# Performance work log

Measured on AMD Instinct MI355X. Metric: run time of the kernel, lower is better.

## Reference

```python
import jax, jax.numpy as jnp
import numpy as np
import math

D = 1024  # output_dim (power of 2)
IN = 1024  # input dim
CAP = int(math.log2(D))  # number of butterfly stages


def _gen_indices(s):
    """Static FFT-butterfly index lists (numpy, computed at trace time)."""
    def ind_s(k):
        if k == 0:
            return [np.array([1, 0])]
        temp = np.arange(2 ** k)
        list0 = [np.concatenate([temp + 2 ** k, temp])]
        list1 = ind_s(k - 1)
        for i in range(k):
            list0.append(np.concatenate([list1[i], list1[i] + 2 ** k]))
        return list0

    t = ind_s(int(math.log2(s // 2)))
    cap = int(math.log2(s))
    ind_exe = [np.asarray(t[i], dtype=np.int32) for i in range(cap)]
    ind_param = []
    for i in range(cap):
        ind = np.concatenate([np.arange(0, s, 2 ** i) + j for j in range(2 ** i)]).astype(np.int32)
        ind_param.append(ind)
    return ind_exe, ind_param


IND_EXE, IND_PARAM = _gen_indices(D)


def setup_inputs() -> dict:
    key = jax.random.key(0)
    ks = jax.random.split(key, 9)
    B = 8192
    x = jax.random.normal(ks[0], (B, IN), dtype=jnp.float32)
    state = jax.random.normal(ks[1], (B, D), dtype=jnp.float32)
    theta = jax.random.uniform(ks[2], (CAP, D // 2), minval=-3.14, maxval=3.14, dtype=jnp.float32)
    U = jax.random.uniform(ks[3], (IN, 3 * D), minval=-0.01, maxval=0.01, dtype=jnp.float32)
    W_r = jax.random.uniform(ks[4], (D, D), minval=-0.01, maxval=0.01, dtype=jnp.float32)
    W_g = jax.random.uniform(ks[5], (D, D), minval=-0.01, maxval=0.01, dtype=jnp.float32)
    bias_r = jnp.full((D,), 2.0, dtype=jnp.float32)
    bias_g = jnp.zeros((D,), dtype=jnp.float32)
    bias_c = jnp.full((D,), 0.01, dtype=jnp.float32)
    return {"x": x, "state": state, "theta": theta, "U": U, "W_r": W_r,
            "W_g": W_g, "bias_r": bias_r, "bias_g": bias_g, "bias_c": bias_c}


def reference(x, state, theta, U, W_r, W_g, bias_r, bias_g, bias_c):
    # fft_param: rotation coefficients, permuted by the static ind_param lists
    cos_list = jnp.concatenate([jnp.cos(theta), jnp.cos(theta)], axis=1)   # [CAP, D]
    sin_list = jnp.concatenate([jnp.sin(theta), -jnp.sin(theta)], axis=1)  # [CAP, D]
    v1 = jnp.stack([cos_list[i][IND_PARAM[i]] for i in range(CAP)])  # [CAP, D]
    v2 = jnp.stack([sin_list[i][IND_PARAM[i]] for i in range(CAP)])  # [CAP, D]

    Ux = x @ U                                   # [B, 3D]
    U_cx, U_rx, U_gx = jnp.split(Ux, 3, axis=1)  # each [B, D]
    r = jax.nn.sigmoid(U_rx + state @ W_r + bias_r)
    g = jax.nn.sigmoid(U_gx + state @ W_g + bias_g)

    # butterfly orthogonal rotation of the state
    h = state
    for i in range(CAP):
        h = h * v1[i] + (h * v2[i])[:, IND_EXE[i]]

    # modReLU
    pre = r * h + U_cx
    c = jnp.sign(pre) * jax.nn.relu(jnp.abs(pre) + 0.001 + bias_c)

    out = g * state + (1.0 - g) * c
    return out
```

## Files before the change

### kernel.cpp

```cpp
#include <hip/hip_runtime.h>
#include <hip/hip_bf16.h>
#include <stdint.h>


typedef __bf16 bf16x8 __attribute__((ext_vector_type(8)));
typedef __bf16 bf16x4 __attribute__((ext_vector_type(4)));
typedef __bf16 bf16x2 __attribute__((ext_vector_type(2)));
typedef float f32x4 __attribute__((ext_vector_type(4)));

#define B_ROWS 8192

__device__ __forceinline__ void async16(__bf16* lds, const __hip_bfloat16* g) {
    __builtin_amdgcn_global_load_lds((const __attribute__((address_space(1))) void*)g,
                                     (__attribute__((address_space(3))) void*)lds,
                                     16, 0, 0);
}

__global__ __launch_bounds__(256) void prep_all(const float* __restrict__ x,
                                                const float* __restrict__ state,
                                                const float* __restrict__ theta,
                                                const float* __restrict__ U,
                                                const float* __restrict__ Wr,
                                                const float* __restrict__ Wg,
                                                __hip_bfloat16* __restrict__ xs,
                                                __hip_bfloat16* __restrict__ Wt0,
                                                __hip_bfloat16* __restrict__ Wt12,
                                                float* __restrict__ v1,
                                                float* __restrict__ v2) {
    __shared__ float tile[32][33];
    const int id = blockIdx.x;
    if (id < 8192) {
        const int row = id;
        const int col = threadIdx.x * 8;
        const float* src = (col < 1024) ? (x + (size_t)row * 1024 + col)
                                        : (state + (size_t)row * 1024 + (col - 1024));
        float4 a = *(const float4*)src;
        float4 b = *(const float4*)(src + 4);
        bf16x8 v;
        v[0] = (__bf16)a.x; v[1] = (__bf16)a.y; v[2] = (__bf16)a.z; v[3] = (__bf16)a.w;
        v[4] = (__bf16)b.x; v[5] = (__bf16)b.y; v[6] = (__bf16)b.z; v[7] = (__bf16)b.w;
        *(bf16x8*)((__bf16*)xs + (size_t)row * 2048 + col) = v;
    } else if (id < 13312) {
        const int wid = id - 8192;
        const float* src; int srcN, scol, sk;
        __hip_bfloat16* dst; int dstStride, dn, dk;
        if (wid < 1024) {
            int nx = wid & 31, ky = wid >> 5;
            src = U; srcN = 3072; scol = nx * 32; sk = ky * 32;
            dst = Wt0; dstStride = 1024; dn = nx * 32; dk = ky * 32;
        } else {
            int id2 = wid - 1024;
            int nx = id2 & 63, ky = id2 >> 6;
            int n0 = nx * 32, k0 = ky * 32;
            dst = Wt12; dstStride = 2048; dn = n0; dk = k0;
            if (k0 < 1024)      { src = U;  srcN = 3072; scol = 1024 + n0; sk = k0; }
            else if (n0 < 1024) { src = Wr; srcN = 1024; scol = n0;        sk = k0 - 1024; }
            else                { src = Wg; srcN = 1024; scol = n0 - 1024; sk = k0 - 1024; }
        }
        const int tx = threadIdx.x & 31, ty = threadIdx.x >> 5;
#pragma unroll
        for (int s = 0; s < 4; ++s)
            tile[ty + s * 8][tx] = src[(size_t)(sk + ty + s * 8) * srcN + scol + tx];
        __syncthreads();
#pragma unroll
        for (int s = 0; s < 4; ++s)
            dst[(size_t)(dn + ty + s * 8) * dstStride + dk + tx] = __float2bfloat16(tile[tx][ty + s * 8]);
    } else {
        int idx = (id - 13312) * 256 + threadIdx.x;
        int i = idx >> 10;
        int j = idx & 1023;
        int Q = 1024 >> i;
        int j0 = j / Q;
        int m = j & (Q - 1);
        int q = (m << i) + j0;
        float th = theta[i * 512 + (q & 511)];
        float c = cosf(th);
        float s = sinf(th);
        v1[idx] = c;
        v2[idx] = (q < 512) ? s : -s;
    }
}

__global__ __launch_bounds__(512, 4) void gemm_fused(const __hip_bfloat16* __restrict__ xs,
                                                     const __hip_bfloat16* __restrict__ Wt0,
                                                     const __hip_bfloat16* __restrict__ Wt12,
                                                     const float* __restrict__ bias_r,
                                                     const float* __restrict__ bias_g,
                                                     __hip_bfloat16* __restrict__ P) {
    __shared__ __align__(16) __bf16 As[128 * 32];
    __shared__ __align__(16) __bf16 Bs1[128 * 32];
    __shared__ __align__(16) __bf16 Bs2[128 * 32];

    const int nt = blockIdx.x;
    const int mt = blockIdx.y;
    const int mBase = mt * 128;

    const int t = threadIdx.x;
    const int lane = t & 63;
    const int wv = t >> 6;
    const int wm = wv & 1;
    const int wn = wv >> 1;
    const int r0 = lane & 15;
    const int gq = lane >> 4;

    const int srow = t >> 2;
    const int sjj = ((t & 3) ^ ((srow >> 1) & 3)) * 8;

    const __hip_bfloat16* A = xs + (size_t)mBase * 2048;

    if (nt < 8) {
        const int c0 = nt * 128;
        const __hip_bfloat16* B1 = Wt12 + (size_t)c0 * 2048;
        const __hip_bfloat16* B2 = Wt12 + (size_t)(1024 + c0) * 2048;

        f32x4 accr[4][2], accg[4][2];
        const f32x4 zero = {0.f, 0.f, 0.f, 0.f};
#pragma unroll
        for (int i = 0; i < 4; ++i)
#pragma unroll
            for (int j = 0; j < 2; ++j) { accr[i][j] = zero; accg[i][j] = zero; }

        for (int k0 = 0; k0 < 2048; k0 += 32) {
            size_t off = (size_t)srow * 2048 + k0 + sjj;
            async16(&As[t * 8], A + off);
            async16(&Bs1[t * 8], B1 + off);
            async16(&Bs2[t * 8], B2 + off);
            __syncthreads();

            bf16x8 af[4], b1[2], b2[2];
#pragma unroll
            for (int i = 0; i < 4; ++i) {
                int row = wm * 64 + i * 16 + r0;
                int cc = row * 4 + (gq ^ ((row >> 1) & 3));
                af[i] = *reinterpret_cast<const bf16x8*>(&As[cc * 8]);
            }
#pragma unroll
            for (int j = 0; j < 2; ++j) {
                int row = wn * 32 + j * 16 + r0;
                int cc = row * 4 + (gq ^ ((row >> 1) & 3));
                b1[j] = *reinterpret_cast<const bf16x8*>(&Bs1[cc * 8]);
                b2[j] = *reinterpret_cast<const bf16x8*>(&Bs2[cc * 8]);
            }
#pragma unroll
            for (int i = 0; i < 4; ++i)
#pragma unroll
                for (int j = 0; j < 2; ++j) {
                    accr[i][j] = __builtin_amdgcn_mfma_f32_16x16x32_bf16(af[i], b1[j], accr[i][j], 0, 0, 0);
                    accg[i][j] = __builtin_amdgcn_mfma_f32_16x16x32_bf16(af[i], b2[j], accg[i][j], 0, 0, 0);
                }
            __syncthreads();
        }

#pragma unroll
        for (int i = 0; i < 4; ++i) {
#pragma unroll
            for (int j = 0; j < 2; ++j) {
#pragma unroll
                for (int reg = 0; reg < 4; ++reg) {
                    int row = mBase + wm * 64 + i * 16 + gq * 4 + reg;
                    int c = c0 + wn * 32 + j * 16 + r0;
                    float zr = 1.0f / (1.0f + __expf(-(accr[i][j][reg] + bias_r[c])));
                    float zg = 1.0f / (1.0f + __expf(-(accg[i][j][reg] + bias_g[c])));
                    bf16x2 pk;
                    pk[0] = (__bf16)zr;
                    pk[1] = (__bf16)zg;
                    *(bf16x2*)((__bf16*)P + (size_t)row * 3072 + 1024 + 2 * c) = pk;
                }
            }
        }
    } else {
        const int c0 = (nt - 8) * 128;
        const __hip_bfloat16* Bb = Wt0 + (size_t)c0 * 1024;

        f32x4 acc[4][2];
        const f32x4 zero = {0.f, 0.f, 0.f, 0.f};
#pragma unroll
        for (int i = 0; i < 4; ++i)
#pragma unroll
            for (int j = 0; j < 2; ++j) acc[i][j] = zero;

        for (int k0 = 0; k0 < 1024; k0 += 32) {
            async16(&As[t * 8], A + (size_t)srow * 2048 + k0 + sjj);
            async16(&Bs1[t * 8], Bb + (size_t)srow * 1024 + k0 + sjj);
            __syncthreads();

            bf16x8 af[4], bf[2];
#pragma unroll
            for (int i = 0; i < 4; ++i) {
                int row = wm * 64 + i * 16 + r0;
                int cc = row * 4 + (gq ^ ((row >> 1) & 3));
                af[i] = *reinterpret_cast<const bf16x8*>(&As[cc * 8]);
            }
#pragma unroll
            for (int j = 0; j < 2; ++j) {
                int row = wn * 32 + j * 16 + r0;
                int cc = row * 4 + (gq ^ ((row >> 1) & 3));
                bf[j] = *reinterpret_cast<const bf16x8*>(&Bs1[cc * 8]);
            }
#pragma unroll
            for (int i = 0; i < 4; ++i)
#pragma unroll
                for (int j = 0; j < 2; ++j)
                    acc[i][j] = __builtin_amdgcn_mfma_f32_16x16x32_bf16(af[i], bf[j], acc[i][j], 0, 0, 0);
            __syncthreads();
        }

#pragma unroll
        for (int i = 0; i < 4; ++i) {
#pragma unroll
            for (int j = 0; j < 2; ++j) {
#pragma unroll
                for (int reg = 0; reg < 4; ++reg) {
                    int row = mBase + wm * 64 + i * 16 + gq * 4 + reg;
                    int c = c0 + wn * 32 + j * 16 + r0;
                    P[(size_t)row * 3072 + c] = __float2bfloat16(acc[i][j][reg]);
                }
            }
        }
    }
}

__global__ __launch_bounds__(256) void fuse_kernel(const float* __restrict__ state,
                                                   const __hip_bfloat16* __restrict__ P,
                                                   const float* __restrict__ v1,
                                                   const float* __restrict__ v2,
                                                   const float* __restrict__ bias_c,
                                                   float* __restrict__ out) {
    __shared__ float hbuf[8][1024];
    const int t = threadIdx.x;
    const int rowBase = blockIdx.x * 8;

    float h[8][4];
    float sv[8][4];
#pragma unroll
    for (int r = 0; r < 8; ++r) {
        float4 s4 = ((const float4*)(state + (size_t)(rowBase + r) * 1024))[t];
        h[r][0] = s4.x; h[r][1] = s4.y; h[r][2] = s4.z; h[r][3] = s4.w;
        sv[r][0] = s4.x; sv[r][1] = s4.y; sv[r][2] = s4.z; sv[r][3] = s4.w;
        *(float4*)&hbuf[r][4 * t] = s4;
    }

    {
        __syncthreads();
        float4 w1 = *(const float4*)&v1[4 * t];
        float4 w2 = *(const float4*)&v2[4 * (t ^ 128)];
        const float w1v[4] = {w1.x, w1.y, w1.z, w1.w};
        const float w2v[4] = {w2.x, w2.y, w2.z, w2.w};
#pragma unroll
        for (int r = 0; r < 8; ++r) {
            float4 pr = *(const float4*)&hbuf[r][4 * (t ^ 128)];
            const float pv[4] = {pr.x, pr.y, pr.z, pr.w};
#pragma unroll
            for (int e = 0; e < 4; ++e) h[r][e] = h[r][e] * w1v[e] + pv[e] * w2v[e];
        }
        __syncthreads();
    }
    {
#pragma unroll
        for (int r = 0; r < 8; ++r)
            *(float4*)&hbuf[r][4 * t] = (float4){h[r][0], h[r][1], h[r][2], h[r][3]};
        __syncthreads();
        float4 w1 = *(const float4*)&v1[1024 + 4 * t];
        float4 w2 = *(const float4*)&v2[1024 + 4 * (t ^ 64)];
        const float w1v[4] = {w1.x, w1.y, w1.z, w1.w};
        const float w2v[4] = {w2.x, w2.y, w2.z, w2.w};
#pragma unroll
        for (int r = 0; r < 8; ++r) {
            float4 pr = *(const float4*)&hbuf[r][4 * (t ^ 64)];
            const float pv[4] = {pr.x, pr.y, pr.z, pr.w};
#pragma unroll
            for (int e = 0; e < 4; ++e) h[r][e] = h[r][e] * w1v[e] + pv[e] * w2v[e];
        }
    }
#pragma unroll
    for (int i = 2; i <= 7; ++i) {
        const int H = 512 >> i;
        const int lm = H >> 2;
        float4 w1 = *(const float4*)&v1[i * 1024 + 4 * t];
        float4 w2 = *(const float4*)&v2[i * 1024 + 4 * (t ^ lm)];
        const float w1v[4] = {w1.x, w1.y, w1.z, w1.w};
        const float w2v[4] = {w2.x, w2.y, w2.z, w2.w};
#pragma unroll
        for (int r = 0; r < 8; ++r) {
#pragma unroll
            for (int e = 0; e < 4; ++e) {
                float p = __shfl_xor(h[r][e], lm, 64);
                h[r][e] = h[r][e] * w1v[e] + p * w2v[e];
            }
        }
    }
    {
        float4 w1 = *(const float4*)&v1[8 * 1024 + 4 * t];
        float4 w2 = *(const float4*)&v2[8 * 1024 + 4 * t];
        const float w1v[4] = {w1.x, w1.y, w1.z, w1.w};
        const float w2v[4] = {w2.x, w2.y, w2.z, w2.w};
#pragma unroll
        for (int r = 0; r < 8; ++r) {
            float nh[4];
#pragma unroll
            for (int e = 0; e < 4; ++e) nh[e] = h[r][e] * w1v[e] + h[r][e ^ 2] * w2v[e ^ 2];
#pragma unroll
            for (int e = 0; e < 4; ++e) h[r][e] = nh[e];
        }
        float4 u1 = *(const float4*)&v1[9 * 1024 + 4 * t];
        float4 u2 = *(const float4*)&v2[9 * 1024 + 4 * t];
        const float u1v[4] = {u1.x, u1.y, u1.z, u1.w};
        const float u2v[4] = {u2.x, u2.y, u2.z, u2.w};
#pragma unroll
        for (int r = 0; r < 8; ++r) {
            float nh[4];
#pragma unroll
            for (int e = 0; e < 4; ++e) nh[e] = h[r][e] * u1v[e] + h[r][e ^ 1] * u2v[e ^ 1];
#pragma unroll
            for (int e = 0; e < 4; ++e) h[r][e] = nh[e];
        }
    }

    const float4 bc = ((const float4*)bias_c)[t];
    const float bcv[4] = {bc.x, bc.y, bc.z, bc.w};
#pragma unroll
    for (int r = 0; r < 8; ++r) {
        const int row = rowBase + r;
        const __hip_bfloat16* Pr = P + (size_t)row * 3072;
        bf16x4 ux = *(const bf16x4*)((const __bf16*)Pr + 4 * t);
        bf16x8 rg = *(const bf16x8*)((const __bf16*)Pr + 1024 + 8 * t);
        float o[4];
#pragma unroll
        for (int e = 0; e < 4; ++e) {
            float Ucx = (float)ux[e];
            float rr  = (float)rg[2 * e];
            float gg  = (float)rg[2 * e + 1];
            float pre = rr * h[r][e] + Ucx;
            float mag = fabsf(pre) + 0.001f + bcv[e];
            float c = (pre > 0.f) ? mag : ((pre < 0.f) ? -mag : 0.f);
            o[e] = gg * sv[r][e] + (1.f - gg) * c;
        }
        ((float4*)(out + (size_t)row * 1024))[t] = (float4){o[0], o[1], o[2], o[3]};
    }
}

extern "C" void kernel_launch(void* const* d_in, const int* in_sizes, int n_in,
                              void* d_out, int out_size, void* d_ws, size_t ws_size,
                              hipStream_t stream) {
    const float* x      = (const float*)d_in[0];
    const float* state  = (const float*)d_in[1];
    const float* theta  = (const float*)d_in[2];
    const float* U      = (const float*)d_in[3];
    const float* W_r    = (const float*)d_in[4];
    const float* W_g    = (const float*)d_in[5];
    const float* bias_r = (const float*)d_in[6];
    const float* bias_g = (const float*)d_in[7];
    const float* bias_c = (const float*)d_in[8];
    float* out = (float*)d_out;

    __hip_bfloat16* xs   = (__hip_bfloat16*)d_ws;
    __hip_bfloat16* Wt0  = xs + (size_t)B_ROWS * 2048;
    __hip_bfloat16* Wt12 = Wt0 + (size_t)1024 * 1024;
    __hip_bfloat16* P    = Wt12 + (size_t)2048 * 2048;
    float* v1 = (float*)(P + (size_t)B_ROWS * 3072);
    float* v2 = v1 + 10 * 1024;

    prep_all<<<13352, 256, 0, stream>>>(x, state, theta, U, W_r, W_g, xs, Wt0, Wt12, v1, v2);
    gemm_fused<<<dim3(16, 64), 512, 0, stream>>>(xs, Wt0, Wt12, bias_r, bias_g, P);
    fuse_kernel<<<1024, 256, 0, stream>>>(state, P, v1, v2, bias_c, out);
}
```

Measured before the change: 282.5 us.

## Fuse fp32-to-bf16 activation conversion into GEMM tile loads

Removes the separate pass that converted x and state to a bf16 staging buffer; the GEMM now reads fp32 activations directly, converts them in registers and writes them into LDS, prefetching the next K slice into registers. This eliminates a full write and re-read of a large intermediate buffer and shrinks the prep launch. In exchange each A tile is fetched as fp32 by every column-tile block, doubling A bytes through L2, and the A path loses the asynchronous global-to-LDS load.

Measured after the change: 320.6 us. 13.5% more time.

```diff
diff --git a/kernel.cpp b/kernel.cpp
--- a/kernel.cpp
+++ b/kernel.cpp
@@ -16,40 +16,25 @@
                                      16, 0, 0);
 }
 
-__global__ __launch_bounds__(256) void prep_all(const float* __restrict__ x,
-                                                const float* __restrict__ state,
-                                                const float* __restrict__ theta,
+__global__ __launch_bounds__(256) void prep_all(const float* __restrict__ theta,
                                                 const float* __restrict__ U,
                                                 const float* __restrict__ Wr,
                                                 const float* __restrict__ Wg,
-                                                __hip_bfloat16* __restrict__ xs,
                                                 __hip_bfloat16* __restrict__ Wt0,
                                                 __hip_bfloat16* __restrict__ Wt12,
                                                 float* __restrict__ v1,
                                                 float* __restrict__ v2) {
     __shared__ float tile[32][33];
     const int id = blockIdx.x;
-    if (id < 8192) {
-        const int row = id;
-        const int col = threadIdx.x * 8;
-        const float* src = (col < 1024) ? (x + (size_t)row * 1024 + col)
-                                        : (state + (size_t)row * 1024 + (col - 1024));
-        float4 a = *(const float4*)src;
-        float4 b = *(const float4*)(src + 4);
-        bf16x8 v;
-        v[0] = (__bf16)a.x; v[1] = (__bf16)a.y; v[2] = (__bf16)a.z; v[3] = (__bf16)a.w;
-        v[4] = (__bf16)b.x; v[5] = (__bf16)b.y; v[6] = (__bf16)b.z; v[7] = (__bf16)b.w;
-        *(bf16x8*)((__bf16*)xs + (size_t)row * 2048 + col) = v;
-    } else if (id < 13312) {
-        const int wid = id - 8192;
+    if (id < 5120) {
         const float* src; int srcN, scol, sk;
         __hip_bfloat16* dst; int dstStride, dn, dk;
-        if (wid < 1024) {
-            int nx = wid & 31, ky = wid >> 5;
+        if (id < 1024) {
+            int nx = id & 31, ky = id >> 5;
             src = U; srcN = 3072; scol = nx * 32; sk = ky * 32;
             dst = Wt0; dstStride = 1024; dn = nx * 32; dk = ky * 32;
         } else {
-            int id2 = wid - 1024;
+            int id2 = id - 1024;
             int nx = id2 & 63, ky = id2 >> 6;
             int n0 = nx * 32, k0 = ky * 32;
             dst = Wt12; dstStride = 2048; dn = n0; dk = k0;
@@ -66,7 +51,7 @@
         for (int s = 0; s < 4; ++s)
             dst[(size_t)(dn + ty + s * 8) * dstStride + dk + tx] = __float2bfloat16(tile[tx][ty + s * 8]);
     } else {
-        int idx = (id - 13312) * 256 + threadIdx.x;
+        int idx = (id - 5120) * 256 + threadIdx.x;
         int i = idx >> 10;
         int j = idx & 1023;
         int Q = 1024 >> i;
@@ -81,7 +66,8 @@
     }
 }
 
-__global__ __launch_bounds__(512, 4) void gemm_fused(const __hip_bfloat16* __restrict__ xs,
+__global__ __launch_bounds__(512, 4) void gemm_fused(const float* __restrict__ x,
+                                                     const float* __restrict__ state,
                                                      const __hip_bfloat16* __restrict__ Wt0,
                                                      const __hip_bfloat16* __restrict__ Wt12,
                                                      const float* __restrict__ bias_r,
@@ -105,8 +91,7 @@
 
     const int srow = t >> 2;
     const int sjj = ((t & 3) ^ ((srow >> 1) & 3)) * 8;
-
-    const __hip_bfloat16* A = xs + (size_t)mBase * 2048;
+    const size_t aRowOff = (size_t)(mBase + srow) * 1024 + sjj;
 
     if (nt < 8) {
         const int c0 = nt * 128;
@@ -120,11 +105,26 @@
 #pragma unroll
             for (int j = 0; j < 2; ++j) { accr[i][j] = zero; accg[i][j] = zero; }
 
+        float4 a0 = *(const float4*)(x + aRowOff);
+        float4 a1 = *(const float4*)(x + aRowOff + 4);
+
         for (int k0 = 0; k0 < 2048; k0 += 32) {
-            size_t off = (size_t)srow * 2048 + k0 + sjj;
-            async16(&As[t * 8], A + off);
-            async16(&Bs1[t * 8], B1 + off);
-            async16(&Bs2[t * 8], B2 + off);
+            size_t offB = (size_t)srow * 2048 + k0 + sjj;
+            async16(&Bs1[t * 8], B1 + offB);
+            async16(&Bs2[t * 8], B2 + offB);
+
+            bf16x8 av;
+            av[0] = (__bf16)a0.x; av[1] = (__bf16)a0.y; av[2] = (__bf16)a0.z; av[3] = (__bf16)a0.w;
+            av[4] = (__bf16)a1.x; av[5] = (__bf16)a1.y; av[6] = (__bf16)a1.z; av[7] = (__bf16)a1.w;
+            *(bf16x8*)&As[t * 8] = av;
+
+            if (k0 + 32 < 2048) {
+                int kn = k0 + 32;
+                const float* srcA = (kn < 1024) ? x : state;
+                size_t offA = aRowOff + (kn & 1023);
+                a0 = *(const float4*)(srcA + offA);
+                a1 = *(const float4*)(srcA + offA + 4);
+            }
             __syncthreads();
 
             bf16x8 af[4], b1[2], b2[2];
@@ -179,9 +179,22 @@
 #pragma unroll
             for (int j = 0; j < 2; ++j) acc[i][j] = zero;
 
+        float4 a0 = *(const float4*)(x + aRowOff);
+        float4 a1 = *(const float4*)(x + aRowOff + 4);
+
         for (int k0 = 0; k0 < 1024; k0 += 32) {
-            async16(&As[t * 8], A + (size_t)srow * 2048 + k0 + sjj);
             async16(&Bs1[t * 8], Bb + (size_t)srow * 1024 + k0 + sjj);
+
+            bf16x8 av;
+            av[0] = (__bf16)a0.x; av[1] = (__bf16)a0.y; av[2] = (__bf16)a0.z; av[3] = (__bf16)a0.w;
+            av[4] = (__bf16)a1.x; av[5] = (__bf16)a1.y; av[6] = (__bf16)a1.z; av[7] = (__bf16)a1.w;
+            *(bf16x8*)&As[t * 8] = av;
+
+            if (k0 + 32 < 1024) {
+                size_t offA = aRowOff + k0 + 32;
+                a0 = *(const float4*)(x + offA);
+                a1 = *(const float4*)(x + offA + 4);
+            }
             __syncthreads();
 
             bf16x8 af[4], bf[2];
@@ -353,14 +366,13 @@
     const float* bias_c = (const float*)d_in[8];
     float* out = (float*)d_out;
 
-    __hip_bfloat16* xs   = (__hip_bfloat16*)d_ws;
-    __hip_bfloat16* Wt0  = xs + (size_t)B_ROWS * 2048;
+    __hip_bfloat16* Wt0  = (__hip_bfloat16*)d_ws;
     __hip_bfloat16* Wt12 = Wt0 + (size_t)1024 * 1024;
     __hip_bfloat16* P    = Wt12 + (size_t)2048 * 2048;
     float* v1 = (float*)(P + (size_t)B_ROWS * 3072);
     float* v2 = v1 + 10 * 1024;
 
-    prep_all<<<13352, 256, 0, stream>>>(x, state, theta, U, W_r, W_g, xs, Wt0, Wt12, v1, v2);
-    gemm_fused<<<dim3(16, 64), 512, 0, stream>>>(xs, Wt0, Wt12, bias_r, bias_g, P);
+    prep_all<<<5160, 256, 0, stream>>>(theta, U, W_r, W_g, Wt0, Wt12, v1, v2);
+    gemm_fused<<<dim3(16, 64), 512, 0, stream>>>(x, state, Wt0, Wt12, bias_r, bias_g, P);
     fuse_kernel<<<1024, 256, 0, stream>>>(state, P, v1, v2, bias_c, out);
 }
```
